# Kernel tuning notes

Measured on AMD Instinct MI355X. Metric: run time of the kernel, lower is better.

## Reference

```python
import jax, jax.numpy as jnp
import numpy as np

N, K, E = 50000, 8, 800000
HID, OUT, DIM_PE, DIM_IN, DIM_EMB = 64, 16, 16, 64, 128

def setup_inputs() -> dict:
    key = jax.random.key(0)
    ks = jax.random.split(key, 16)
    s = 0.05
    inp = {
        "eigvecs": jax.random.normal(ks[0], (N, K), jnp.float32),
        "x": jax.random.normal(ks[1], (N, DIM_IN), jnp.float32),
        "edge_index": jax.random.randint(ks[2], (2, E), 0, N, jnp.int32),
        "batch_index": jnp.sort(jax.random.randint(ks[3], (N,), 0, 8, jnp.int32)),
        # GIN layer 0: MLP(1 -> HID, 1 layer) == single Linear
        "W0": jax.random.normal(ks[4], (1, HID), jnp.float32) * s,
        "b0": jnp.zeros((HID,), jnp.float32),
        # GIN layer 1: MLP(HID -> HID, 1 layer)
        "W1": jax.random.normal(ks[5], (HID, HID), jnp.float32) * s,
        "b1": jnp.zeros((HID,), jnp.float32),
        # GIN layer 2: MLP(HID -> HID -> OUT, 2 layers, relu between)
        "W2a": jax.random.normal(ks[6], (HID, HID), jnp.float32) * s,
        "b2a": jnp.zeros((HID,), jnp.float32),
        "W2b": jax.random.normal(ks[7], (HID, OUT), jnp.float32) * s,
        "b2b": jnp.zeros((OUT,), jnp.float32),
        # rho: MLP(OUT*K -> HID -> DIM_PE, 2 layers)
        "Wr1": jax.random.normal(ks[8], (OUT * K, HID), jnp.float32) * s,
        "br1": jnp.zeros((HID,), jnp.float32),
        "Wr2": jax.random.normal(ks[9], (HID, DIM_PE), jnp.float32) * s,
        "br2": jnp.zeros((DIM_PE,), jnp.float32),
        # linear_x: dim_in -> dim_emb - dim_pe
        "Wx": jax.random.normal(ks[10], (DIM_IN, DIM_EMB - DIM_PE), jnp.float32) * s,
        "bx": jnp.zeros((DIM_EMB - DIM_PE,), jnp.float32),
    }
    return inp

def reference(eigvecs, x, edge_index, batch_index,
              W0, b0, W1, b1, W2a, b2a, W2b, b2b,
              Wr1, br1, Wr2, br2, Wx, bx):
    src, dst = edge_index[0], edge_index[1]

    def agg(h):
        # GINConv sum aggregation: out[i] = h[i] + sum_{(j->i) in E} h[j]  (eps=0)
        return h + jax.ops.segment_sum(h[src], dst, num_segments=N)

    def enc(p):
        # p: [N, K, C]; Linear acts on last dim, message passing on node dim 0
        h = agg(p) @ W0 + b0                       # GINConv(MLP 1-layer): [N,K,HID]
        h = agg(h) @ W1 + b1                       # GINConv(MLP 1-layer)
        m = agg(h)
        return jax.nn.relu(m @ W2a + b2a) @ W2b + b2b  # GINConv(MLP 2-layer): [N,K,OUT]

    # pos_enc = eigvecs.unsqueeze(-1), NaN -> 0
    pos = jnp.nan_to_num(eigvecs)[:, :, None]      # [N,K,1]
    pe = enc(pos) + enc(-pos)                      # sign-invariant sum: [N,K,OUT]
    pe = pe.reshape(N, K * OUT)                    # [N, K*OUT]
    pe = jax.nn.relu(pe @ Wr1 + br1) @ Wr2 + br2   # rho MLP: [N, DIM_PE]

    h = x.astype(jnp.float32) @ Wx + bx            # expand_x linear: [N, DIM_EMB-DIM_PE]
    return jnp.concatenate([h, pe], axis=1)        # [N, DIM_EMB]
```

## Files before the change

### kernel.cpp

```cpp
#include <hip/hip_runtime.h>

__global__ void zero_k(int* __restrict__ p, int n) {
  int i = blockIdx.x * blockDim.x + threadIdx.x;
  if (i < n) p[i] = 0;
}

__global__ void hist_k(const int* __restrict__ ei, int* __restrict__ cnt, int E) {
  int e = blockIdx.x * blockDim.x + threadIdx.x;
  if (e < E) atomicAdd(&cnt[ei[E + e]], 1);
}

__global__ void scan_k(int* __restrict__ ptr, int* __restrict__ cur, int N,
                       const float* __restrict__ W0, const float* __restrict__ b0,
                       const float* __restrict__ W1, const float* __restrict__ b1,
                       const float* __restrict__ W2a, float* __restrict__ SV) {
  __shared__ int sums[256];
  __shared__ float w01[64], g[64];
  int t = threadIdx.x;
  int chunk = (N + 255) / 256;
  int lo = t * chunk, hi = lo + chunk; if (hi > N) hi = N; if (lo > N) lo = N;
  int s = 0;
  for (int i = lo; i < hi; ++i) s += ptr[i];
  sums[t] = s;
  if (t < 64) {
    float a = 0.f, bg = 0.f;
    for (int i = 0; i < 64; ++i) { float w = W1[i*64 + t]; a += W0[i]*w; bg += b0[i]*w; }
    w01[t] = a; g[t] = bg;
  }
  __syncthreads();
  for (int off = 1; off < 256; off <<= 1) {
    int v = (t >= off) ? sums[t - off] : 0;
    __syncthreads();
    sums[t] += v;
    __syncthreads();
  }
  int run = sums[t] - s;
  for (int i = lo; i < hi; ++i) {
    int c = ptr[i];
    ptr[i] = run; cur[i] = run;
    run += c;
  }
  if (t == 255) ptr[N] = run;
  if (t < 64) {
    float w012 = 0.f, P = 0.f, Q = 0.f;
    for (int i = 0; i < 64; ++i) { float w = W2a[i*64 + t]; w012 += w01[i]*w; P += g[i]*w; Q += b1[i]*w; }
    SV[t] = w012; SV[64 + t] = P; SV[128 + t] = Q;
  }
}

__global__ void fill_k(const int* __restrict__ ei, int* __restrict__ cur,
                       int* __restrict__ csr, int E) {
  int e = blockIdx.x * blockDim.x + threadIdx.x;
  if (e >= E) return;
  int s = ei[e], d = ei[E + e];
  int pos = atomicAdd(&cur[d], 1);
  csr[pos] = s;
}

#define RED16(v) { v += __shfl_down(v, 8, 16); v += __shfl_down(v, 4, 16); \
                   v += __shfl_down(v, 2, 16); v += __shfl_down(v, 1, 16); }
#define NANFIX4(u) { u.x = (u.x!=u.x)?0.f:u.x; u.y = (u.y!=u.y)?0.f:u.y; \
                     u.z = (u.z!=u.z)?0.f:u.z; u.w = (u.w!=u.w)?0.f:u.w; }

template<int MODE>
__global__ __launch_bounds__(256) void aggv_k(
    const int* __restrict__ ptr, const int* __restrict__ csr,
    const float* __restrict__ Fin, const float* __restrict__ Din,
    float* __restrict__ Fout, float* __restrict__ Dout, int N) {
  int g = blockIdx.x * 16 + (threadIdx.x >> 4);
  int t = threadIdx.x & 15;
  if (g >= N) return;
  int lo = ptr[g], hi = ptr[g + 1];
  float a0=0.f,a1=0.f,a2=0.f,a3=0.f,a4=0.f,a5=0.f,a6=0.f,a7=0.f,dd=0.f;
  for (int j = lo + t; j < hi; j += 16) {
    int s = csr[j];
    const float* r = Fin + (size_t)s * 8;
    float4 u0 = *(const float4*)r;
    float4 u1 = *(const float4*)(r + 4);
    if (MODE == 0) { NANFIX4(u0); NANFIX4(u1); }
    a0 += u0.x; a1 += u0.y; a2 += u0.z; a3 += u0.w;
    a4 += u1.x; a5 += u1.y; a6 += u1.z; a7 += u1.w;
    if (MODE == 1) dd += Din[s];
  }
  RED16(a0); RED16(a1); RED16(a2); RED16(a3);
  RED16(a4); RED16(a5); RED16(a6); RED16(a7);
  if (MODE == 1) RED16(dd);
  if (t == 0) {
    const float* r = Fin + (size_t)g * 8;
    float4 s0 = *(const float4*)r;
    float4 s1 = *(const float4*)(r + 4);
    if (MODE == 0) { NANFIX4(s0); NANFIX4(s1); }
    float4 o0 = { a0 + s0.x, a1 + s0.y, a2 + s0.z, a3 + s0.w };
    float4 o1 = { a4 + s1.x, a5 + s1.y, a6 + s1.z, a7 + s1.w };
    *(float4*)(Fout + (size_t)g * 8)     = o0;
    *(float4*)(Fout + (size_t)g * 8 + 4) = o1;
    if (MODE == 0) Dout[g] = 1.f + (float)(hi - lo);
    if (MODE == 1) Dout[g] = Din[g] + dd;
  }
}

__global__ __launch_bounds__(256) void pe_k(
    const float* __restrict__ B3, const float* __restrict__ D1, const float* __restrict__ D2,
    const float* __restrict__ SV, const float* __restrict__ b2a,
    const float* __restrict__ W2b, const float* __restrict__ b2b,
    const float* __restrict__ Wr1, const float* __restrict__ br1,
    const float* __restrict__ Wr2, const float* __restrict__ br2,
    const float* __restrict__ x, const float* __restrict__ Wx,
    const float* __restrict__ bx,
    float* __restrict__ out, int N) {
  __shared__ float w2bT[16][68];
  __shared__ float wr2T[16][68];
  __shared__ float vbuf[4][8][68];
  __shared__ float pebuf[16][128];
  __shared__ float zbuf[16][68];
  int tid = threadIdx.x;
  int wid = tid >> 6, lane = tid & 63;

  for (int u = tid; u < 1024; u += 256) {
    int j = u >> 4, o = u & 15;
    w2bT[o][j] = W2b[u];
    wr2T[o][j] = Wr2[u];
  }
  __syncthreads();

  int nb = blockIdx.x * 16 + wid * 4;
  float w012 = SV[lane], P = SV[64 + lane], Q = SV[128 + lane], b2aj = b2a[lane];
  int o16 = lane & 15, kk = lane >> 4;
  float bb2 = 2.f * b2b[o16];
  float br1h = br1[lane];

  #pragma unroll
  for (int m = 0; m < 4; ++m) {
    int n = nb + m;
    int nc = (n < N) ? n : 0;
    float d1 = D1[nc], d2 = D2[nc];
    float E = fmaf(d2, P, fmaf(d1, Q, b2aj));
    float E2 = E + E;
    const float* srow = B3 + (size_t)nc * 8;
    #pragma unroll
    for (int k = 0; k < 8; ++k) {
      float t = srow[k] * w012;
      vbuf[wid][k][lane] = fmaxf(fmaxf(E2, E + fabsf(t)), 0.f);
    }
    float accA = bb2, accB = bb2;
    #pragma unroll
    for (int j4 = 0; j4 < 16; ++j4) {
      float4 w4 = *(const float4*)&w2bT[o16][4 * j4];
      float4 va = *(const float4*)&vbuf[wid][kk][4 * j4];
      float4 vb = *(const float4*)&vbuf[wid][kk + 4][4 * j4];
      accA += va.x * w4.x + va.y * w4.y + va.z * w4.z + va.w * w4.w;
      accB += vb.x * w4.x + vb.y * w4.y + vb.z * w4.z + vb.w * w4.w;
    }
    pebuf[wid * 4 + m][lane]      = accA;
    pebuf[wid * 4 + m][lane + 64] = accB;
  }

  float za[4] = { br1h, br1h, br1h, br1h };
  #pragma unroll 8
  for (int c4 = 0; c4 < 32; ++c4) {
    float w0 = Wr1[(4 * c4 + 0) * 64 + lane];
    float w1 = Wr1[(4 * c4 + 1) * 64 + lane];
    float w2 = Wr1[(4 * c4 + 2) * 64 + lane];
    float w3 = Wr1[(4 * c4 + 3) * 64 + lane];
    #pragma unroll
    for (int m = 0; m < 4; ++m) {
      float4 p = *(const float4*)&pebuf[wid * 4 + m][4 * c4];
      za[m] += p.x * w0 + p.y * w1 + p.z * w2 + p.w * w3;
    }
  }
  #pragma unroll
  for (int m = 0; m < 4; ++m) zbuf[wid * 4 + m][lane] = fmaxf(za[m], 0.f);

  float acc2 = br2[o16];
  #pragma unroll
  for (int h4 = 0; h4 < 16; ++h4) {
    float4 zv = *(const float4*)&zbuf[wid * 4 + kk][4 * h4];
    float4 wv = *(const float4*)&wr2T[o16][4 * h4];
    acc2 += zv.x * wv.x + zv.y * wv.y + zv.z * wv.z + zv.w * wv.w;
  }
  {
    int nn = nb + kk;
    if (nn < N) out[(size_t)nn * 128 + 112 + o16] = acc2;
  }

  float bxa = bx[lane];
  float bxb = (lane < 48) ? bx[lane + 64] : 0.f;
  float xacc[4][2];
  #pragma unroll
  for (int m = 0; m < 4; ++m) { xacc[m][0] = bxa; xacc[m][1] = bxb; }
  #pragma unroll 4
  for (int i4 = 0; i4 < 16; ++i4) {
    float4 xv[4];
    #pragma unroll
    for (int m = 0; m < 4; ++m) {
      int nc = (nb + m < N) ? (nb + m) : 0;
      xv[m] = *(const float4*)(x + (size_t)nc * 64 + 4 * i4);
    }
    #pragma unroll
    for (int i = 0; i < 4; ++i) {
      int row = 4 * i4 + i;
      float wa = Wx[row * 112 + lane];
      float wb = (lane < 48) ? Wx[row * 112 + lane + 64] : 0.f;
      #pragma unroll
      for (int m = 0; m < 4; ++m) {
        float xs = ((const float*)&xv[m])[i];
        xacc[m][0] = fmaf(xs, wa, xacc[m][0]);
        xacc[m][1] = fmaf(xs, wb, xacc[m][1]);
      }
    }
  }
  #pragma unroll
  for (int m = 0; m < 4; ++m) {
    int n = nb + m;
    if (n < N) {
      out[(size_t)n * 128 + lane] = xacc[m][0];
      if (lane < 48) out[(size_t)n * 128 + lane + 64] = xacc[m][1];
    }
  }
}

extern "C" void kernel_launch(void* const* d_in, const int* in_sizes, int n_in,
                              void* d_out, int out_size, void* d_ws, size_t ws_size,
                              hipStream_t stream) {
  const float* eig = (const float*)d_in[0];
  const float* x   = (const float*)d_in[1];
  const int*   ei  = (const int*)d_in[2];
  const float* W0  = (const float*)d_in[4];
  const float* b0  = (const float*)d_in[5];
  const float* W1  = (const float*)d_in[6];
  const float* b1  = (const float*)d_in[7];
  const float* W2a = (const float*)d_in[8];
  const float* b2a = (const float*)d_in[9];
  const float* W2b = (const float*)d_in[10];
  const float* b2b = (const float*)d_in[11];
  const float* Wr1 = (const float*)d_in[12];
  const float* br1 = (const float*)d_in[13];
  const float* Wr2 = (const float*)d_in[14];
  const float* br2 = (const float*)d_in[15];
  const float* Wx  = (const float*)d_in[16];
  const float* bx  = (const float*)d_in[17];
  float* out = (float*)d_out;

  int N = in_sizes[0] / 8;
  int E = in_sizes[2] / 2;

  int* ptr = (int*)d_ws;
  int* cur = ptr + (N + 1);
  int* csr = cur + N;
  uintptr_t p = (uintptr_t)(csr + E);
  p = (p + 255) & ~(uintptr_t)255;
  float* B1 = (float*)p;
  float* B2 = B1 + (size_t)N * 8;
  float* B3 = B2 + (size_t)N * 8;
  float* D1 = B3 + (size_t)N * 8;
  float* D2 = D1 + N;
  float* SV = D2 + N;

  int eblocks = (E + 255) / 256;
  int nblocks16 = (N + 15) / 16;

  zero_k<<<(N + 256) / 256, 256, 0, stream>>>(ptr, N + 1);
  hist_k<<<eblocks, 256, 0, stream>>>(ei, ptr, E);
  scan_k<<<1, 256, 0, stream>>>(ptr, cur, N, W0, b0, W1, b1, W2a, SV);
  fill_k<<<eblocks, 256, 0, stream>>>(ei, cur, csr, E);

  aggv_k<0><<<nblocks16, 256, 0, stream>>>(ptr, csr, eig, nullptr, B1, D1, N);
  aggv_k<1><<<nblocks16, 256, 0, stream>>>(ptr, csr, B1, D1, B2, D2, N);
  aggv_k<2><<<nblocks16, 256, 0, stream>>>(ptr, csr, B2, nullptr, B3, nullptr, N);

  pe_k<<<nblocks16, 256, 0, stream>>>(B3, D1, D2, SV, b2a, W2b, b2b,
                                      Wr1, br1, Wr2, br2, x, Wx, bx, out, N);
}
```

Measured before the change: 472.0 us.

## Fold W2b into Wr1 and compute dense stage one node per thread

Precomputes a combined matrix M = W2b·Wr1 for each of the 8 eigenvector slots, plus a constant bias C0, so the OUT=16 intermediate and one GEMM stage disappear. The dense epilogue kernel is rewritten so each thread handles one node with register accumulators and packed 2-wide FMAs, reading weights as uniform broadcasts instead of staging through shared memory. Per node the FLOPs grow (8×64×64 instead of 8×64×16 + 128×64), and the large per-thread register arrays risk spills and low occupancy with 64-thread blocks.

```diff
diff --git a/kernel.cpp b/kernel.cpp
--- a/kernel.cpp
+++ b/kernel.cpp
@@ -1,4 +1,6 @@
 #include <hip/hip_runtime.h>
+
+typedef float v2f __attribute__((ext_vector_type(2)));
 
 __global__ void zero_k(int* __restrict__ p, int n) {
   int i = blockIdx.x * blockDim.x + threadIdx.x;
@@ -10,10 +12,23 @@
   if (e < E) atomicAdd(&cnt[ei[E + e]], 1);
 }
 
+__global__ void mk_k(const float* __restrict__ W2b, const float* __restrict__ Wr1,
+                     float* __restrict__ M) {
+  int idx = blockIdx.x * 256 + threadIdx.x;
+  int k = idx >> 12, j = (idx >> 6) & 63, h = idx & 63;
+  float m = 0.f;
+  #pragma unroll
+  for (int o = 0; o < 16; ++o) m = fmaf(W2b[j*16 + o], Wr1[(k*16 + o)*64 + h], m);
+  M[idx] = m;
+}
+
 __global__ void scan_k(int* __restrict__ ptr, int* __restrict__ cur, int N,
                        const float* __restrict__ W0, const float* __restrict__ b0,
                        const float* __restrict__ W1, const float* __restrict__ b1,
-                       const float* __restrict__ W2a, float* __restrict__ SV) {
+                       const float* __restrict__ W2a, const float* __restrict__ b2a,
+                       const float* __restrict__ b2b, const float* __restrict__ br1,
+                       const float* __restrict__ Wr1,
+                       float4* __restrict__ SV4, float* __restrict__ C0) {
   __shared__ int sums[256];
   __shared__ float w01[64], g[64];
   int t = threadIdx.x;
@@ -44,7 +59,16 @@
   if (t < 64) {
     float w012 = 0.f, P = 0.f, Q = 0.f;
     for (int i = 0; i < 64; ++i) { float w = W2a[i*64 + t]; w012 += w01[i]*w; P += g[i]*w; Q += b1[i]*w; }
-    SV[t] = w012; SV[64 + t] = P; SV[128 + t] = Q;
+    float4 sv; sv.x = w012; sv.y = P; sv.z = Q; sv.w = b2a[t];
+    SV4[t] = sv;
+    float c0 = br1[t];
+    for (int o = 0; o < 16; ++o) {
+      float srow = 0.f;
+      #pragma unroll
+      for (int k = 0; k < 8; ++k) srow += Wr1[(k*16 + o)*64 + t];
+      c0 = fmaf(2.f * b2b[o], srow, c0);
+    }
+    C0[t] = c0;
   }
 }
 
@@ -99,122 +123,90 @@
   }
 }
 
-__global__ __launch_bounds__(256) void pe_k(
+__global__ __launch_bounds__(64) void dense_k(
     const float* __restrict__ B3, const float* __restrict__ D1, const float* __restrict__ D2,
-    const float* __restrict__ SV, const float* __restrict__ b2a,
-    const float* __restrict__ W2b, const float* __restrict__ b2b,
-    const float* __restrict__ Wr1, const float* __restrict__ br1,
+    const float4* __restrict__ SV4, const float* __restrict__ C0,
+    const float* __restrict__ M,
     const float* __restrict__ Wr2, const float* __restrict__ br2,
     const float* __restrict__ x, const float* __restrict__ Wx,
     const float* __restrict__ bx,
     float* __restrict__ out, int N) {
-  __shared__ float w2bT[16][68];
-  __shared__ float wr2T[16][68];
-  __shared__ float vbuf[4][8][68];
-  __shared__ float pebuf[16][128];
-  __shared__ float zbuf[16][68];
-  int tid = threadIdx.x;
-  int wid = tid >> 6, lane = tid & 63;
-
-  for (int u = tid; u < 1024; u += 256) {
-    int j = u >> 4, o = u & 15;
-    w2bT[o][j] = W2b[u];
-    wr2T[o][j] = Wr2[u];
-  }
-  __syncthreads();
-
-  int nb = blockIdx.x * 16 + wid * 4;
-  float w012 = SV[lane], P = SV[64 + lane], Q = SV[128 + lane], b2aj = b2a[lane];
-  int o16 = lane & 15, kk = lane >> 4;
-  float bb2 = 2.f * b2b[o16];
-  float br1h = br1[lane];
-
-  #pragma unroll
-  for (int m = 0; m < 4; ++m) {
-    int n = nb + m;
-    int nc = (n < N) ? n : 0;
-    float d1 = D1[nc], d2 = D2[nc];
-    float E = fmaf(d2, P, fmaf(d1, Q, b2aj));
-    float E2 = E + E;
-    const float* srow = B3 + (size_t)nc * 8;
+  int n = blockIdx.x * 64 + threadIdx.x;
+  bool act = (n < N);
+  int nc = act ? n : 0;
+  float d1 = D1[nc], d2 = D2[nc];
+  float4 s0 = *(const float4*)(B3 + (size_t)nc * 8);
+  float4 s1 = *(const float4*)(B3 + (size_t)nc * 8 + 4);
+  float s[8] = { s0.x, s0.y, s0.z, s0.w, s1.x, s1.y, s1.z, s1.w };
+
+  v2f z[32];
+  const v2f* c0p = (const v2f*)C0;
+  #pragma unroll
+  for (int h2 = 0; h2 < 32; ++h2) z[h2] = c0p[h2];
+
+  #pragma unroll
+  for (int k = 0; k < 8; ++k) {
+    float sk = s[k];
+    const v2f* Mk = (const v2f*)(M + (size_t)k * 64 * 64);
+    #pragma unroll 2
+    for (int j = 0; j < 64; ++j) {
+      float4 sv = SV4[j];
+      float E = fmaf(d2, sv.y, fmaf(d1, sv.z, sv.w));
+      float t = sk * sv.x;
+      float v = fmaxf(fmaxf(E + E, E + fabsf(t)), 0.f);
+      v2f vv; vv.x = v; vv.y = v;
+      const v2f* mrow = Mk + j * 32;
+      #pragma unroll
+      for (int h2 = 0; h2 < 32; ++h2) z[h2] += vv * mrow[h2];
+    }
+  }
+
+  v2f o2[8];
+  const v2f* br2p = (const v2f*)br2;
+  #pragma unroll
+  for (int q = 0; q < 8; ++q) o2[q] = br2p[q];
+  #pragma unroll
+  for (int h = 0; h < 64; ++h) {
+    float zh = (h & 1) ? z[h >> 1].y : z[h >> 1].x;
+    zh = fmaxf(zh, 0.f);
+    v2f vv; vv.x = zh; vv.y = zh;
+    const v2f* wrow = (const v2f*)(Wr2 + h * 16);
     #pragma unroll
-    for (int k = 0; k < 8; ++k) {
-      float t = srow[k] * w012;
-      vbuf[wid][k][lane] = fmaxf(fmaxf(E2, E + fabsf(t)), 0.f);
-    }
-    float accA = bb2, accB = bb2;
+    for (int q = 0; q < 8; ++q) o2[q] += vv * wrow[q];
+  }
+  if (act) {
+    float4* op = (float4*)(out + (size_t)n * 128 + 112);
     #pragma unroll
-    for (int j4 = 0; j4 < 16; ++j4) {
-      float4 w4 = *(const float4*)&w2bT[o16][4 * j4];
-      float4 va = *(const float4*)&vbuf[wid][kk][4 * j4];
-      float4 vb = *(const float4*)&vbuf[wid][kk + 4][4 * j4];
-      accA += va.x * w4.x + va.y * w4.y + va.z * w4.z + va.w * w4.w;
-      accB += vb.x * w4.x + vb.y * w4.y + vb.z * w4.z + vb.w * w4.w;
-    }
-    pebuf[wid * 4 + m][lane]      = accA;
-    pebuf[wid * 4 + m][lane + 64] = accB;
-  }
-
-  float za[4] = { br1h, br1h, br1h, br1h };
-  #pragma unroll 8
-  for (int c4 = 0; c4 < 32; ++c4) {
-    float w0 = Wr1[(4 * c4 + 0) * 64 + lane];
-    float w1 = Wr1[(4 * c4 + 1) * 64 + lane];
-    float w2 = Wr1[(4 * c4 + 2) * 64 + lane];
-    float w3 = Wr1[(4 * c4 + 3) * 64 + lane];
+    for (int q4 = 0; q4 < 4; ++q4) {
+      float4 st; st.x = o2[2*q4].x; st.y = o2[2*q4].y; st.z = o2[2*q4+1].x; st.w = o2[2*q4+1].y;
+      op[q4] = st;
+    }
+  }
+
+  const float4* xr4 = (const float4*)(x + (size_t)nc * 64);
+  for (int half = 0; half < 2; ++half) {
+    v2f acc[28];
+    const v2f* bxp = (const v2f*)(bx + half * 56);
     #pragma unroll
-    for (int m = 0; m < 4; ++m) {
-      float4 p = *(const float4*)&pebuf[wid * 4 + m][4 * c4];
-      za[m] += p.x * w0 + p.y * w1 + p.z * w2 + p.w * w3;
-    }
-  }
-  #pragma unroll
-  for (int m = 0; m < 4; ++m) zbuf[wid * 4 + m][lane] = fmaxf(za[m], 0.f);
-
-  float acc2 = br2[o16];
-  #pragma unroll
-  for (int h4 = 0; h4 < 16; ++h4) {
-    float4 zv = *(const float4*)&zbuf[wid * 4 + kk][4 * h4];
-    float4 wv = *(const float4*)&wr2T[o16][4 * h4];
-    acc2 += zv.x * wv.x + zv.y * wv.y + zv.z * wv.z + zv.w * wv.w;
-  }
-  {
-    int nn = nb + kk;
-    if (nn < N) out[(size_t)nn * 128 + 112 + o16] = acc2;
-  }
-
-  float bxa = bx[lane];
-  float bxb = (lane < 48) ? bx[lane + 64] : 0.f;
-  float xacc[4][2];
-  #pragma unroll
-  for (int m = 0; m < 4; ++m) { xacc[m][0] = bxa; xacc[m][1] = bxb; }
-  #pragma unroll 4
-  for (int i4 = 0; i4 < 16; ++i4) {
-    float4 xv[4];
-    #pragma unroll
-    for (int m = 0; m < 4; ++m) {
-      int nc = (nb + m < N) ? (nb + m) : 0;
-      xv[m] = *(const float4*)(x + (size_t)nc * 64 + 4 * i4);
-    }
-    #pragma unroll
-    for (int i = 0; i < 4; ++i) {
-      int row = 4 * i4 + i;
-      float wa = Wx[row * 112 + lane];
-      float wb = (lane < 48) ? Wx[row * 112 + lane + 64] : 0.f;
-      #pragma unroll
-      for (int m = 0; m < 4; ++m) {
-        float xs = ((const float*)&xv[m])[i];
-        xacc[m][0] = fmaf(xs, wa, xacc[m][0]);
-        xacc[m][1] = fmaf(xs, wb, xacc[m][1]);
+    for (int q = 0; q < 28; ++q) acc[q] = bxp[q];
+    for (int i4 = 0; i4 < 16; ++i4) {
+      float4 xv = xr4[i4];
+      #pragma unroll
+      for (int c = 0; c < 4; ++c) {
+        float xs = (c == 0) ? xv.x : (c == 1) ? xv.y : (c == 2) ? xv.z : xv.w;
+        v2f vv; vv.x = xs; vv.y = xs;
+        const v2f* wrow = (const v2f*)(Wx + (i4 * 4 + c) * 112 + half * 56);
+        #pragma unroll
+        for (int q = 0; q < 28; ++q) acc[q] += vv * wrow[q];
       }
     }
-  }
-  #pragma unroll
-  for (int m = 0; m < 4; ++m) {
-    int n = nb + m;
-    if (n < N) {
-      out[(size_t)n * 128 + lane] = xacc[m][0];
-      if (lane < 48) out[(size_t)n * 128 + lane + 64] = xacc[m][1];
+    if (act) {
+      float4* op = (float4*)(out + (size_t)n * 128 + half * 56);
+      #pragma unroll
+      for (int q4 = 0; q4 < 14; ++q4) {
+        float4 st; st.x = acc[2*q4].x; st.y = acc[2*q4].y; st.z = acc[2*q4+1].x; st.w = acc[2*q4+1].y;
+        op[q4] = st;
+      }
     }
   }
 }
@@ -249,25 +241,29 @@
   int* csr = cur + N;
   uintptr_t p = (uintptr_t)(csr + E);
   p = (p + 255) & ~(uintptr_t)255;
-  float* B1 = (float*)p;
-  float* B2 = B1 + (size_t)N * 8;
-  float* B3 = B2 + (size_t)N * 8;
-  float* D1 = B3 + (size_t)N * 8;
-  float* D2 = D1 + N;
-  float* SV = D2 + N;
+  float* B1  = (float*)p;
+  float* B2  = B1 + (size_t)N * 8;
+  float* B3  = B2 + (size_t)N * 8;
+  float* D1  = B3 + (size_t)N * 8;
+  float* D2  = D1 + N;
+  float* SV4 = D2 + N;
+  float* C0  = SV4 + 256;
+  float* M   = C0 + 64;
 
   int eblocks = (E + 255) / 256;
   int nblocks16 = (N + 15) / 16;
 
   zero_k<<<(N + 256) / 256, 256, 0, stream>>>(ptr, N + 1);
+  mk_k<<<128, 256, 0, stream>>>(W2b, Wr1, M);
   hist_k<<<eblocks, 256, 0, stream>>>(ei, ptr, E);
-  scan_k<<<1, 256, 0, stream>>>(ptr, cur, N, W0, b0, W1, b1, W2a, SV);
+  scan_k<<<1, 256, 0, stream>>>(ptr, cur, N, W0, b0, W1, b1, W2a,
+                                b2a, b2b, br1, Wr1, (float4*)SV4, C0);
   fill_k<<<eblocks, 256, 0, stream>>>(ei, cur, csr, E);
 
   aggv_k<0><<<nblocks16, 256, 0, stream>>>(ptr, csr, eig, nullptr, B1, D1, N);
   aggv_k<1><<<nblocks16, 256, 0, stream>>>(ptr, csr, B1, D1, B2, D2, N);
   aggv_k<2><<<nblocks16, 256, 0, stream>>>(ptr, csr, B2, nullptr, B3, nullptr, N);
 
-  pe_k<<<nblocks16, 256, 0, stream>>>(B3, D1, D2, SV, b2a, W2b, b2b,
-                                      Wr1, br1, Wr2, br2, x, Wx, bx, out, N);
-}
+  dense_k<<<(N + 63) / 64, 64, 0, stream>>>(B3, D1, D2, (const float4*)SV4, C0, M,
+                                            Wr2, br2, x, Wx, bx, out, N);
+}
```

Result: slower. 535.4 us (+13.4%).
